# Kernel optimization log

Measured on AMD Instinct MI355X. Metric: run time of the kernel, lower is better.

The kernel has to match this reference:

```python
import jax, jax.numpy as jnp
import numpy as np


def setup_inputs() -> dict:
    key = jax.random.key(0)
    ks = jax.random.split(key, 20)
    B, T, N, Cin = 1, 12, 30000, 16
    H, Hc = 64, 128
    O, KW = 12, 128
    E2 = 480000  # half of edges; symmetrized below -> E = 960000
    s = 0.05
    node_features = jax.random.normal(ks[0], (B, T, N, Cin), jnp.float32)
    src = jax.random.randint(ks[1], (T, E2), 0, N)
    dst = jax.random.randint(ks[2], (T, E2), 0, N)
    edge_index = jnp.concatenate(
        [jnp.stack([src, dst], axis=1), jnp.stack([dst, src], axis=1)], axis=-1)  # [T,2,E]
    return dict(
        node_features=node_features,
        edge_index=edge_index,
        gru_Wih0=jax.random.normal(ks[3], (2, 3 * H, Cin), jnp.float32) * s,
        gru_Whh0=jax.random.normal(ks[4], (2, 3 * H, H), jnp.float32) * s,
        gru_bih0=jax.random.normal(ks[5], (2, 3 * H), jnp.float32) * s,
        gru_bhh0=jax.random.normal(ks[6], (2, 3 * H), jnp.float32) * s,
        gru_Wih1=jax.random.normal(ks[7], (2, 3 * H, 2 * H), jnp.float32) * s,
        gru_Whh1=jax.random.normal(ks[8], (2, 3 * H, H), jnp.float32) * s,
        gru_bih1=jax.random.normal(ks[9], (2, 3 * H), jnp.float32) * s,
        gru_bhh1=jax.random.normal(ks[10], (2, 3 * H), jnp.float32) * s,
        ln_scale=jnp.ones((H,), jnp.float32),
        ln_bias=jnp.zeros((H,), jnp.float32),
        cheb_W=jax.random.normal(ks[11], (3, H, Hc), jnp.float32) * s,
        cheb_b=jnp.zeros((Hc,), jnp.float32),
        conv_W=jax.random.normal(ks[12], (O, T, 1, KW), jnp.float32) * s,
        conv_b=jnp.zeros((O,), jnp.float32),
    )


def reference(node_features, edge_index, gru_Wih0, gru_Whh0, gru_bih0, gru_bhh0,
              gru_Wih1, gru_Whh1, gru_bih1, gru_bhh1, ln_scale, ln_bias,
              cheb_W, cheb_b, conv_W, conv_b):
    B, T, N, Cin = node_features.shape
    H = gru_Whh0.shape[-1]
    M = B * N
    x = node_features.transpose(0, 2, 1, 3).reshape(M, T, Cin)

    def bigru(x, Wih, Whh, bih, bhh):
        # PyTorch bidirectional GRU layer (eval mode -> no dropout)
        outs = []
        for d, rev in ((0, False), (1, True)):
            gi = jnp.einsum('mtd,gd->tmg', x, Wih[d]) + bih[d]  # [T, M, 3H]
            def step(h, g, d=d):
                gh = h @ Whh[d].T + bhh[d]
                ir, iz, inn = jnp.split(g, 3, axis=-1)
                hr, hz, hn = jnp.split(gh, 3, axis=-1)
                r = jax.nn.sigmoid(ir + hr)
                z = jax.nn.sigmoid(iz + hz)
                n = jnp.tanh(inn + r * hn)
                h = (1.0 - z) * n + z * h
                return h, h
            h0 = jnp.zeros((x.shape[0], Whh.shape[-1]), x.dtype)
            _, ys = jax.lax.scan(step, h0, gi, reverse=rev)
            outs.append(jnp.swapaxes(ys, 0, 1))
        return jnp.concatenate(outs, axis=-1)  # [M, T, 2H]

    x = bigru(x, gru_Wih0, gru_Whh0, gru_bih0, gru_bhh0)
    x = bigru(x, gru_Wih1, gru_Whh1, gru_bih1, gru_bhh1)
    # reshape(M,T,2,H), LayerNorm(H), take direction 1 == slice then LayerNorm
    xb = x[:, :, H:]
    mu = jnp.mean(xb, axis=-1, keepdims=True)
    var = jnp.mean((xb - mu) ** 2, axis=-1, keepdims=True)
    xb = (xb - mu) * jax.lax.rsqrt(var + 1e-5) * ln_scale + ln_bias
    xs_t = jnp.moveaxis(xb.reshape(B, N, T, H), 2, 0).reshape(T, M, H)  # per-timestep [M,H]

    E = edge_index.shape[-1]
    N_ITER = 75  # power-iteration steps for lambda_max (scipy eigs equivalent)

    def cheb_step(_, inp):
        x_t, edges = inp  # x_t [M,H], edges [2,E]
        row, col = edges[0], edges[1]
        deg = jax.ops.segment_sum(jnp.ones((E,), x_t.dtype), row, num_segments=M)
        def Lmv(v):  # unnormalized Laplacian (D - A) matvec
            return deg * v - jax.ops.segment_sum(v[col], row, num_segments=M)
        v0 = jnp.full((M,), 1.0 / np.sqrt(M), x_t.dtype)
        def pit(i, v):
            w = Lmv(v)
            return w / (jnp.linalg.norm(w) + 1e-12)
        v = jax.lax.fori_loop(0, N_ITER, pit, v0)
        lam = jnp.vdot(v, Lmv(v))  # lambda_max of D - A (LaplacianLambdaMax default)
        # ChebConv sym-normalized, rescaled Laplacian: L_hat = (2/lam)*(I - D^-1/2 A D^-1/2) - I
        dinv = jnp.where(deg > 0, 1.0 / jnp.sqrt(jnp.maximum(deg, 1.0)), 0.0)
        we = (-2.0 / lam) * dinv[row] * dinv[col]  # off-diagonal weights
        diag = 2.0 / lam - 1.0                      # diagonal (all nodes)
        def Lhat(xm):
            return diag * xm + jax.ops.segment_sum(we[:, None] * xm[col], row, num_segments=M)
        Tx0 = x_t
        Tx1 = Lhat(Tx0)
        Tx2 = 2.0 * Lhat(Tx1) - Tx0
        out = Tx0 @ cheb_W[0] + Tx1 @ cheb_W[1] + Tx2 @ cheb_W[2] + cheb_b
        return 0, out

    _, emb = jax.lax.scan(cheb_step, 0, (xs_t, edge_index))  # [T, M, Hc]
    Hc = cheb_W.shape[-1]
    emb = jnp.moveaxis(emb.reshape(T, B, N, Hc), 0, 1)  # [B, T, N, Hc]
    # Conv2d(T -> O, kernel (1,KW)) followed by [:,:,:,-1]: only last window matters
    KW = conv_W.shape[-1]
    out = jnp.einsum('btnk,otk->bno', emb[..., Hc - KW:], conv_W[:, :, 0, :]) + conv_b
    return jax.nn.sigmoid(out)  # [B, N, num_for_predict]
```

## Files before the change

kernel.cpp:

```cpp
#include <hip/hip_runtime.h>
#include <hip/hip_bf16.h>

#define DEV __device__ __forceinline__

constexpr int Mn  = 30000;
constexpr int Tt  = 12;
constexpr int CIN = 16;
constexpr int Hh  = 64;
constexpr int Gg  = 192;
constexpr int C2  = 128;
constexpr int Ee  = 960000;
constexpr int HC  = 128;
constexpr int Oo  = 12;
constexpr int KW  = 128;
constexpr int SEGS= 938;
constexpr int NB  = 235;
constexpr int EPB = 8192;
constexpr int BPT = 118;
constexpr int CHK = 21;
constexpr int RC  = 1440;
constexpr int NRND= 76;
constexpr int NF4A= 21*256;
constexpr int NF4B= 20*104 + 44;

DEV float bf2f(__hip_bfloat16 v){ return __bfloat162float(v); }
DEV __hip_bfloat16 f2bf(float v){ return __float2bfloat16(v); }
DEV float sigm(float x){ return __builtin_amdgcn_rcpf(1.f + __expf(-x)); }
DEV float tanh_f(float x){ return 1.f - 2.f*__builtin_amdgcn_rcpf(__expf(2.f*x) + 1.f); }

DEV float aload_f(const float* p){ return __hip_atomic_load(p, __ATOMIC_RELAXED, __HIP_MEMORY_SCOPE_AGENT); }
DEV void  astore_f(float* p, float v){ __hip_atomic_store(p, v, __ATOMIC_RELAXED, __HIP_MEMORY_SCOPE_AGENT); }
DEV int   aload_i(const int* p){ return __hip_atomic_load(p, __ATOMIC_RELAXED, __HIP_MEMORY_SCOPE_AGENT); }
DEV void  astore_i(int* p, int v){ __hip_atomic_store(p, v, __ATOMIC_RELAXED, __HIP_MEMORY_SCOPE_AGENT); }
DEV unsigned long long aload_u64(const unsigned long long* p){ return __hip_atomic_load(p, __ATOMIC_RELAXED, __HIP_MEMORY_SCOPE_AGENT); }
DEV void astore_u64(unsigned long long* p, unsigned long long v){ __hip_atomic_store(p, v, __ATOMIC_RELAXED, __HIP_MEMORY_SCOPE_AGENT); }

typedef short bfrag8 __attribute__((ext_vector_type(8)));
typedef float ffrag4 __attribute__((ext_vector_type(4)));

DEV int off_h(int row, int col){
  return row*64 + ((((col >> 3) ^ (row & 7)) << 3) | (col & 7));
}

DEV short bfbits(float v){ __hip_bfloat16 b = f2bf(v); return *reinterpret_cast<short*>(&b); }

__global__ void k_init(int* bcnt, int* bfill, int* flagA, unsigned long long* pbB){
  int i = blockIdx.x*256 + threadIdx.x;
  if (i < Tt*CHK*16){ flagA[i] = 0; pbB[i] = 0ull; }
  if (i < Tt*NB){ bcnt[i] = 0; bfill[i] = 0; }
}

__global__ __launch_bounds__(256) void k_bcnt(const int* __restrict__ ei, int* __restrict__ bcnt){
  __shared__ int h[NB];
  const int b = blockIdx.x;
  const int w = (b & 7)*177 + (b >> 3);
  const int t = w / BPT, ch = w - t*BPT;
  const int e0 = ch*EPB;
  const int tid = threadIdx.x;
  for (int i = tid; i < NB; i += 256) h[i] = 0;
  __syncthreads();
  #pragma unroll
  for (int i = 0; i < 32; ++i){
    int e = e0 + i*256 + tid;
    if (e < Ee){
      int r = ei[(size_t)(t*2)*Ee + e];
      atomicAdd(&h[r >> 7], 1);
    }
  }
  __syncthreads();
  for (int i = tid; i < NB; i += 256){
    int c = h[i];
    if (c > 0) atomicAdd(&bcnt[t*NB + i], c);
  }
}

__global__ __launch_bounds__(256) void k_bscan(const int* __restrict__ bcnt, int* __restrict__ rpb){
  int t = blockIdx.x, tid = threadIdx.x;
  __shared__ int ps[256];
  int v = (tid < NB) ? bcnt[t*NB + tid] : 0;
  ps[tid] = v;
  __syncthreads();
  for (int o = 1; o < 256; o <<= 1){
    int x = (tid >= o) ? ps[tid-o] : 0;
    __syncthreads();
    ps[tid] += x;
    __syncthreads();
  }
  if (tid < NB) rpb[t*(NB+1) + tid] = ps[tid] - v;
  if (tid == 255) rpb[t*(NB+1) + NB] = ps[NB-1];
}

__global__ __launch_bounds__(256) void k_part2(const int* __restrict__ ei, const int* __restrict__ rpb,
    int* __restrict__ bfill, unsigned* __restrict__ pair){
  __shared__ int hcnt[NB];
  __shared__ int hbase[NB];
  const int b = blockIdx.x;
  const int w = (b & 7)*177 + (b >> 3);
  const int t = w / BPT, ch = w - t*BPT;
  const int e0 = ch*EPB;
  const int tid = threadIdx.x;
  for (int i = tid; i < NB; i += 256) hcnt[i] = 0;
  __syncthreads();
  unsigned key[32];
  #pragma unroll
  for (int i = 0; i < 32; ++i){
    int e = e0 + i*256 + tid;
    unsigned k = 0xFFFFFFFFu;
    if (e < Ee){
      int r = ei[(size_t)(t*2)*Ee + e];
      int c = ei[(size_t)(t*2+1)*Ee + e];
      k = ((unsigned)r << 16) | (unsigned)c;
      atomicAdd(&hcnt[r >> 7], 1);
    }
    key[i] = k;
  }
  __syncthreads();
  for (int i = tid; i < NB; i += 256){
    int cnt = hcnt[i];
    int base = (cnt > 0) ? atomicAdd(&bfill[t*NB + i], cnt) : 0;
    hbase[i] = rpb[t*(NB+1) + i] + base;
  }
  __syncthreads();
  for (int i = tid; i < NB; i += 256) hcnt[i] = 0;
  __syncthreads();
  #pragma unroll
  for (int i = 0; i < 32; ++i){
    unsigned k = key[i];
    if (k != 0xFFFFFFFFu){
      int r = (int)(k >> 16);
      int bk = r >> 7;
      int pos = atomicAdd(&hcnt[bk], 1);
      pair[(size_t)t*Ee + hbase[bk] + pos] = ((unsigned)(r & 127) << 16) | (k & 0xFFFFu);
    }
  }
}

__global__ __launch_bounds__(256) void k_csr2(const int* __restrict__ rpb, const unsigned* __restrict__ pair,
    unsigned short* __restrict__ col16, int* __restrict__ rp, float* __restrict__ dinv){
  __shared__ unsigned short cols_s[9216];
  __shared__ int lcnt[128], lfill[128];
  __shared__ int ps[256];
  const int blk = blockIdx.x;
  const int t = blk / NB, bk = blk - t*NB;
  const int r0 = bk << 7;
  const int nr = (r0 + 128 <= Mn) ? 128 : (Mn - r0);
  const int base = rpb[t*(NB+1) + bk];
  const int cnt  = rpb[t*(NB+1) + bk + 1] - base;
  const int tid = threadIdx.x;
  if (tid < 128) lcnt[tid] = 0;
  __syncthreads();
  for (int i = tid; i < cnt; i += 256){
    unsigned v = pair[(size_t)t*Ee + base + i];
    atomicAdd(&lcnt[v >> 16], 1);
  }
  __syncthreads();
  int v2 = (tid < 128) ? lcnt[tid] : 0;
  ps[tid] = v2;
  __syncthreads();
  for (int o = 1; o < 128; o <<= 1){
    int x = (tid >= o) ? ps[tid-o] : 0;
    __syncthreads();
    ps[tid] += x;
    __syncthreads();
  }
  if (tid < 128){
    int excl = ps[tid] - v2;
    lfill[tid] = excl;
    if (tid < nr){
      rp[t*(Mn+1) + r0 + tid] = base + excl;
      dinv[t*Mn + r0 + tid] = (v2 > 0) ? rsqrtf((float)v2) : 0.f;
    }
  }
  if (bk == NB-1 && tid == 0) rp[t*(Mn+1) + Mn] = base + cnt;
  __syncthreads();
  for (int i = tid; i < cnt; i += 256){
    unsigned v = pair[(size_t)t*Ee + base + i];
    int pos = atomicAdd(&lfill[v >> 16], 1);
    cols_s[pos] = (unsigned short)(v & 0xFFFFu);
  }
  __syncthreads();
  for (int i = tid; i < cnt; i += 256)
    col16[(size_t)t*Ee + base + i] = cols_s[i];
}

__global__ __launch_bounds__(1024) void k_perm(const int* __restrict__ rp, int* __restrict__ prow){
  __shared__ int hist[256], hbase[256], ps[256];
  const int b = blockIdx.x;
  const int t = b / CHK, ch = b - t*CHK;
  const int r0 = ch*RC;
  const int r1 = (r0 + RC < Mn) ? r0 + RC : Mn;
  const int n = r1 - r0;
  const int tid = threadIdx.x;
  if (tid < 256) hist[tid] = 0;
  __syncthreads();
  const int* rpt = rp + t*(Mn+1);
  int d0 = -1, d1 = -1;
  if (tid < n){ int m = r0 + tid; d0 = min(rpt[m+1]-rpt[m], 255); atomicAdd(&hist[d0], 1); }
  if (1024 + tid < n){ int m = r0 + 1024 + tid; d1 = min(rpt[m+1]-rpt[m], 255); atomicAdd(&hist[d1], 1); }
  __syncthreads();
  if (tid < 256) ps[tid] = hist[tid];
  __syncthreads();
  for (int o = 1; o < 256; o <<= 1){
    int x = (tid >= o && tid < 256) ? ps[tid-o] : 0;
    __syncthreads();
    if (tid < 256) ps[tid] += x;
    __syncthreads();
  }
  if (tid < 256){ hbase[tid] = ps[tid] - hist[tid]; hist[tid] = 0; }
  __syncthreads();
  if (d0 >= 0){ int pos = hbase[d0] + atomicAdd(&hist[d0], 1); prow[(size_t)b*RC + pos] = r0 + tid; }
  if (d1 >= 0){ int pos = hbase[d1] + atomicAdd(&hist[d1], 1); prow[(size_t)b*RC + pos] = r0 + 1024 + tid; }
}

__global__ __launch_bounds__(256) void k_gru0(
    const float* __restrict__ nf, const float* __restrict__ Wih, const float* __restrict__ Whh,
    const float* __restrict__ bih, const float* __restrict__ bhh, __hip_bfloat16* __restrict__ y0)
{
  __shared__ __hip_bfloat16 xp[Tt*32*32];
  __shared__ __hip_bfloat16 h_hi[32*64];
  __shared__ __hip_bfloat16 h_lo[32*64];
  const int tid = threadIdx.x;
  const int m0  = blockIdx.x*32;
  const int lane = tid & 63, wv = tid >> 6;
  const int lr = lane & 15, lq = lane >> 4;
  for (int idx = tid; idx < Tt*32*CIN; idx += 256){
    int t = idx >> 9; int row = (idx >> 4) & 31; int k = idx & 15;
    int m = m0 + row;
    float v = (m < Mn) ? nf[((size_t)t*Mn + m)*CIN + k] : 0.f;
    __hip_bfloat16 hi = f2bf(v);
    xp[(t*32 + row)*32 + k]      = hi;
    xp[(t*32 + row)*32 + 16 + k] = f2bf(v - bf2f(hi));
  }
  for (int d = 0; d < 2; ++d){
    bfrag8 Bh[3][2], Bx[3];
    float b_r, b_z, b_in, b_hn;
    {
      const float* Wh = Whh + (size_t)d*Gg*Hh;
      const float* Wx = Wih + (size_t)d*Gg*CIN;
      #pragma unroll
      for (int c = 0; c < 3; ++c){
        int g = (wv + 4*c)*16 + lr;
        #pragma unroll
        for (int ks = 0; ks < 2; ++ks){
          bfrag8 f;
          #pragma unroll
          for (int r = 0; r < 8; ++r) f[r] = bfbits(Wh[(size_t)g*Hh + ks*32 + lq*8 + r]);
          Bh[c][ks] = f;
        }
        bfrag8 fx;
        #pragma unroll
        for (int r = 0; r < 8; ++r) fx[r] = bfbits(Wx[(size_t)g*CIN + ((lq*8 + r) & 15)]);
        Bx[c] = fx;
      }
      int j = wv*16 + lr;
      b_r  = bih[d*Gg + j]        + bhh[d*Gg + j];
      b_z  = bih[d*Gg + Hh + j]   + bhh[d*Gg + Hh + j];
      b_in = bih[d*Gg + 2*Hh + j];
      b_hn = bhh[d*Gg + 2*Hh + j];
    }
    float hreg[8];
    #pragma unroll
    for (int q = 0; q < 8; ++q) hreg[q] = 0.f;
    for (int i = tid; i < 32*64; i += 256){ h_hi[i] = f2bf(0.f); h_lo[i] = f2bf(0.f); }
    __syncthreads();
    for (int step = 0; step < Tt; ++step){
      int t = d ? (Tt-1-step) : step;
      bfrag8 xa[2], hhf[2][2], hlf[2][2];
      #pragma unroll
      for (int rt = 0; rt < 2; ++rt){
        int row = rt*16 + lr;
        xa[rt] = *(const bfrag8*)&xp[(t*32 + row)*32 + lq*8];
        #pragma unroll
        for (int ks = 0; ks < 2; ++ks){
          int e = off_h(row, ks*32 + lq*8);
          hhf[rt][ks] = *(const bfrag8*)&h_hi[e];
          hlf[rt][ks] = *(const bfrag8*)&h_lo[e];
        }
      }
      ffrag4 Cr[2], Cz[2], Cai[2], Cah[2];
      #pragma unroll
      for (int rt = 0; rt < 2; ++rt){
        ffrag4 z4 = (ffrag4){0.f,0.f,0.f,0.f};
        Cr[rt]  = __builtin_amdgcn_mfma_f32_16x16x32_bf16(xa[rt], Bx[0], z4, 0,0,0);
        Cz[rt]  = __builtin_amdgcn_mfma_f32_16x16x32_bf16(xa[rt], Bx[1], z4, 0,0,0);
        Cai[rt] = __builtin_amdgcn_mfma_f32_16x16x32_bf16(xa[rt], Bx[2], z4, 0,0,0);
        Cah[rt] = z4;
        #pragma unroll
        for (int ks = 0; ks < 2; ++ks){
          Cr[rt]  = __builtin_amdgcn_mfma_f32_16x16x32_bf16(hhf[rt][ks], Bh[0][ks], Cr[rt], 0,0,0);
          Cr[rt]  = __builtin_amdgcn_mfma_f32_16x16x32_bf16(hlf[rt][ks], Bh[0][ks], Cr[rt], 0,0,0);
          Cz[rt]  = __builtin_amdgcn_mfma_f32_16x16x32_bf16(hhf[rt][ks], Bh[1][ks], Cz[rt], 0,0,0);
          Cz[rt]  = __builtin_amdgcn_mfma_f32_16x16x32_bf16(hlf[rt][ks], Bh[1][ks], Cz[rt], 0,0,0);
          Cah[rt] = __builtin_amdgcn_mfma_f32_16x16x32_bf16(hhf[rt][ks], Bh[2][ks], Cah[rt], 0,0,0);
          Cah[rt] = __builtin_amdgcn_mfma_f32_16x16x32_bf16(hlf[rt][ks], Bh[2][ks], Cah[rt], 0,0,0);
        }
      }
      __syncthreads();
      #pragma unroll
      for (int rt = 0; rt < 2; ++rt){
        #pragma unroll
        for (int q = 0; q < 4; ++q){
          float r = sigm(Cr[rt][q] + b_r);
          float z = sigm(Cz[rt][q] + b_z);
          float n = tanh_f((Cai[rt][q] + b_in) + r*(Cah[rt][q] + b_hn));
          float h = (1.f - z)*n + z*hreg[rt*4+q];
          hreg[rt*4+q] = h;
          __hip_bfloat16 hi = f2bf(h);
          int e = off_h(rt*16 + lq*4 + q, wv*16 + lr);
          h_hi[e] = hi;
          h_lo[e] = f2bf(h - bf2f(hi));
        }
      }
      __syncthreads();
      {
        int row = tid >> 3, cg = tid & 7;
        int m = m0 + row;
        if (m < Mn){
          float4 v = *(const float4*)&h_hi[off_h(row, cg*8)];
          *(float4*)&y0[((size_t)t*Mn + m)*C2 + d*Hh + cg*8] = v;
        }
      }
    }
    __syncthreads();
  }
}

__global__ void k_wcvt(const float* __restrict__ W, __hip_bfloat16* __restrict__ Wbf){
  int i = blockIdx.x*256 + threadIdx.x;
  if (i < Gg*C2) Wbf[i] = f2bf(W[i]);
}

__global__ __launch_bounds__(256) void k_gru1r(const __hip_bfloat16* __restrict__ y0,
    const __hip_bfloat16* __restrict__ Wbf, const float* __restrict__ Whh,
    const float* __restrict__ bih, const float* __restrict__ bhh,
    const float* __restrict__ lns, const float* __restrict__ lnb,
    __hip_bfloat16* __restrict__ xbt)
{
  __shared__ __hip_bfloat16 h_hi[32*64];
  __shared__ __hip_bfloat16 h_lo[32*64];
  __shared__ float h_f32[32*72];
  __shared__ float sc[Hh], bs[Hh];
  const int tid = threadIdx.x;
  const int seg = blockIdx.x;
  const int m0  = seg*32;
  const int lane = tid & 63, wv = tid >> 6;
  const int lr = lane & 15, lq = lane >> 4;
  bfrag8 Bh[3][2];
  #pragma unroll
  for (int c = 0; c < 3; ++c){
    int g = (wv + 4*c)*16 + lr;
    #pragma unroll
    for (int ks = 0; ks < 2; ++ks){
      bfrag8 f;
      #pragma unroll
      for (int r = 0; r < 8; ++r) f[r] = bfbits(Whh[(size_t)g*Hh + ks*32 + lq*8 + r]);
      Bh[c][ks] = f;
    }
  }
  bfrag8 Bp[3][4];
  #pragma unroll
  for (int c = 0; c < 3; ++c){
    int g = (wv + 4*c)*16 + lr;
    #pragma unroll
    for (int ks = 0; ks < 4; ++ks)
      Bp[c][ks] = *(const bfrag8*)(Wbf + (size_t)g*C2 + ks*32 + lq*8);
  }
  float b_r, b_z, b_in, b_hn;
  {
    int j = wv*16 + lr;
    b_r  = bih[j]      + bhh[j];
    b_z  = bih[Hh+j]   + bhh[Hh+j];
    b_in = bih[2*Hh+j];
    b_hn = bhh[2*Hh+j];
  }
  if (tid < Hh){ sc[tid] = lns[tid]; bs[tid] = lnb[tid]; }
  float hreg[8];
  #pragma unroll
  for (int q = 0; q < 8; ++q) hreg[q] = 0.f;
  for (int i = tid; i < 32*64; i += 256){ h_hi[i] = f2bf(0.f); h_lo[i] = f2bf(0.f); }
  __syncthreads();
  for (int step = 0; step < Tt; ++step){
    int t = Tt-1-step;
    const __hip_bfloat16* yb = y0 + (size_t)t*Mn*C2;
    ffrag4 Cr[2], Cz[2], Cai[2], Cah[2];
    #pragma unroll
    for (int rt = 0; rt < 2; ++rt){
      ffrag4 z4 = (ffrag4){0.f,0.f,0.f,0.f};
      Cr[rt] = z4; Cz[rt] = z4; Cai[rt] = z4; Cah[rt] = z4;
    }
    #pragma unroll
    for (int ks = 0; ks < 4; ++ks){
      const int ko = ks*32 + lq*8;
      bfrag8 a0 = *(const bfrag8*)(yb + (size_t)(m0 + lr     )*C2 + ko);
      bfrag8 a1 = *(const bfrag8*)(yb + (size_t)(m0 + 16 + lr)*C2 + ko);
      Cr[0]  = __builtin_amdgcn_mfma_f32_16x16x32_bf16(a0, Bp[0][ks], Cr[0], 0,0,0);
      Cr[1]  = __builtin_amdgcn_mfma_f32_16x16x32_bf16(a1, Bp[0][ks], Cr[1], 0,0,0);
      Cz[0]  = __builtin_amdgcn_mfma_f32_16x16x32_bf16(a0, Bp[1][ks], Cz[0], 0,0,0);
      Cz[1]  = __builtin_amdgcn_mfma_f32_16x16x32_bf16(a1, Bp[1][ks], Cz[1], 0,0,0);
      Cai[0] = __builtin_amdgcn_mfma_f32_16x16x32_bf16(a0, Bp[2][ks], Cai[0], 0,0,0);
      Cai[1] = __builtin_amdgcn_mfma_f32_16x16x32_bf16(a1, Bp[2][ks], Cai[1], 0,0,0);
    }
    bfrag8 hhf[2][2], hlf[2][2];
    #pragma unroll
    for (int rt = 0; rt < 2; ++rt){
      int row = rt*16 + lr;
      #pragma unroll
      for (int ks = 0; ks < 2; ++ks){
        int e = off_h(row, ks*32 + lq*8);
        hhf[rt][ks] = *(const bfrag8*)&h_hi[e];
        hlf[rt][ks] = *(const bfrag8*)&h_lo[e];
      }
    }
    #pragma unroll
    for (int rt = 0; rt < 2; ++rt){
      #pragma unroll
      for (int ks = 0; ks < 2; ++ks){
        Cr[rt]  = __builtin_amdgcn_mfma_f32_16x16x32_bf16(hhf[rt][ks], Bh[0][ks], Cr[rt], 0,0,0);
        Cr[rt]  = __builtin_amdgcn_mfma_f32_16x16x32_bf16(hlf[rt][ks], Bh[0][ks], Cr[rt], 0,0,0);
        Cz[rt]  = __builtin_amdgcn_mfma_f32_16x16x32_bf16(hhf[rt][ks], Bh[1][ks], Cz[rt], 0,0,0);
        Cz[rt]  = __builtin_amdgcn_mfma_f32_16x16x32_bf16(hlf[rt][ks], Bh[1][ks], Cz[rt], 0,0,0);
        Cah[rt] = __builtin_amdgcn_mfma_f32_16x16x32_bf16(hhf[rt][ks], Bh[2][ks], Cah[rt], 0,0,0);
        Cah[rt] = __builtin_amdgcn_mfma_f32_16x16x32_bf16(hlf[rt][ks], Bh[2][ks], Cah[rt], 0,0,0);
      }
    }
    __syncthreads();
    #pragma unroll
    for (int rt = 0; rt < 2; ++rt){
      #pragma unroll
      for (int q = 0; q < 4; ++q){
        float r = sigm(Cr[rt][q] + b_r);
        float z = sigm(Cz[rt][q] + b_z);
        float n = tanh_f((Cai[rt][q] + b_in) + r*(Cah[rt][q] + b_hn));
        float h = (1.f - z)*n + z*hreg[rt*4+q];
        hreg[rt*4+q] = h;
        __hip_bfloat16 hi = f2bf(h);
        int row = rt*16 + lq*4 + q;
        int e = off_h(row, wv*16 + lr);
        h_hi[e] = hi;
        h_lo[e] = f2bf(h - bf2f(hi));
        h_f32[row*72 + wv*16 + lr] = h;
      }
    }
    __syncthreads();
    {
      int row = tid >> 3, l = tid & 7;
      float4 v0 = *(const float4*)&h_f32[row*72 + l*8];
      float4 v1 = *(const float4*)&h_f32[row*72 + l*8 + 4];
      float vals[8] = {v0.x, v0.y, v0.z, v0.w, v1.x, v1.y, v1.z, v1.w};
      float s1 = 0.f, s2 = 0.f;
      #pragma unroll
      for (int q = 0; q < 8; ++q){ s1 += vals[q]; s2 += vals[q]*vals[q]; }
      #pragma unroll
      for (int off = 1; off <= 4; off <<= 1){ s1 += __shfl_xor(s1, off); s2 += __shfl_xor(s2, off); }
      float mu  = s1 * (1.f/64.f);
      float var = s2 * (1.f/64.f) - mu*mu;
      float rs  = rsqrtf(var + 1e-5f);
      int m = m0 + row;
      if (m < Mn){
        __hip_bfloat16 ob[8];
        #pragma unroll
        for (int q = 0; q < 8; ++q){ int j = l*8 + q; ob[q] = f2bf((vals[q]-mu)*rs*sc[j] + bs[j]); }
        *(float4*)&xbt[((size_t)t*Mn + m)*Hh + l*8] = *(float4*)ob;
      }
    }
    __syncthreads();
  }
}

__global__ __launch_bounds__(1024) void k_pitall(const int* __restrict__ rp,
    const unsigned short* __restrict__ col, float* __restrict__ urb,
    int* __restrict__ flagA, unsigned long long* __restrict__ pbB,
    float* __restrict__ lamc, const int* __restrict__ prow, int rA, int rB)
{
  __shared__ alignas(16) float u_s[Mn];
  __shared__ float redw[16];
  __shared__ float s_nrm;
  __shared__ int s_goA, s_goB;
  const int b = blockIdx.x;
  const int t = b / CHK, ch = b - t*CHK;
  const int r0 = ch*RC;
  const int r1 = (r0 + RC < Mn) ? r0 + RC : Mn;
  const int n = r1 - r0;
  const int tid = threadIdx.x;
  const int lane = tid & 63;
  const int wv   = tid >> 6;
  const unsigned short* cp = col + (size_t)t*Ee;
  const int fS = t*CHK*16;
  const int pB = t*CHK*16;
  const int* pr = prow + (size_t)b*RC;
  const int rowA = (tid < n)        ? pr[tid]        : -1;
  const int rowB = (1024 + tid < n) ? pr[1024 + tid] : -1;
  int rb0 = 0, re0 = 0, rb1 = 0, re1 = 0;
  {
    const int* rpt = rp + t*(Mn+1);
    if (rowA >= 0){ rb0 = rpt[rowA]; re0 = rpt[rowA+1]; }
    if (rowB >= 0){ rb1 = rpt[rowB]; re1 = rpt[rowB+1]; }
  }
  if (tid == 0){ s_nrm = 1.0f; s_goA = 0; s_goB = 0; }
  __syncthreads();
  for (int r = rA; r <= rB; ++r){
    const int fin = (r == NRND);
    if (r == 1){
      for (int i = tid; i < Mn; i += 1024) u_s[i] = 0.005773502691896258f;
    } else {
      const int rr = r - 1;
      const float4* u4 = (const float4*)(urb + (size_t)rr*(Tt*Mn) + (size_t)t*Mn);
      float4* s4 = (float4*)u_s;
      if (wv == 0){
        const bool mine = lane < CHK;
        for (;;){ int v = mine ? aload_i(&flagA[fS + lane*16]) : 0x7FFFFFFF;
                  if (__all(v >= rr)) break; __builtin_amdgcn_s_sleep(4); }
        if (lane == 0) __hip_atomic_store(&s_goA, rr, __ATOMIC_RELAXED, __HIP_MEMORY_SCOPE_WORKGROUP);
      } else {
        while (__hip_atomic_load(&s_goA, __ATOMIC_RELAXED, __HIP_MEMORY_SCOPE_WORKGROUP) < rr)
          __builtin_amdgcn_s_sleep(2);
      }
      asm volatile("" ::: "memory");
      for (int i = tid; i < NF4A; i += 1024){
        int idx = (i >> 8)*360 + (i & 255);
        s4[idx] = u4[idx];
      }
      unsigned long long pv = 0;
      if (wv == 0){
        const bool mine = lane < CHK;
        for (;;){ pv = mine ? aload_u64(&pbB[(size_t)(pB + lane*16) + (rr & 1)*8])
                            : ((unsigned long long)rr << 32);
                  if (__all((int)(pv >> 32) == rr)) break; __builtin_amdgcn_s_sleep(4); }
        if (lane == 0) __hip_atomic_store(&s_goB, rr, __ATOMIC_RELAXED, __HIP_MEMORY_SCOPE_WORKGROUP);
      } else {
        while (__hip_atomic_load(&s_goB, __ATOMIC_RELAXED, __HIP_MEMORY_SCOPE_WORKGROUP) < rr)
          __builtin_amdgcn_s_sleep(2);
      }
      asm volatile("" ::: "memory");
      for (int i = tid; i < NF4B; i += 1024){
        int ck = i/104, off = i - ck*104;
        int idx = ck*360 + 256 + off;
        s4[idx] = u4[idx];
      }
      if (wv == 0){
        float p = (lane < CHK) ? __uint_as_float((unsigned)pv) : 0.f;
        #pragma unroll
        for (int o2 = 1; o2 < 32; o2 <<= 1) p += __shfl_xor(p, o2);
        if (tid == 0) s_nrm = p;
      }
    }
    __syncthreads();
    const float inv_s = fin ? 1.f : 1.f/(sqrtf(s_nrm) + 1e-12f);
    float* u_ot = urb + (size_t)r*(Tt*Mn);
    float local = 0.f;
    if (rowA >= 0){
      float s = 0.f;
      int i = rb0;
      for (; i < re0 && (i & 3); ++i) s += u_s[cp[i]];
      for (; i + 4 <= re0; i += 4){
        ushort4 c4 = *(const ushort4*)(cp + i);
        s += (u_s[c4.x] + u_s[c4.y]) + (u_s[c4.z] + u_s[c4.w]);
      }
      for (; i < re0; ++i) s += u_s[cp[i]];
      float uv = u_s[rowA];
      float wv2 = (float)(re0 - rb0)*uv - s;
      if (!fin){ float o = inv_s*wv2; astore_f(&u_ot[t*Mn + rowA], o); local += o*o; }
      else local += uv*wv2;
    }
    asm volatile("s_waitcnt vmcnt(0)" ::: "memory");
    __syncthreads();
    if (tid == 0) astore_i(&flagA[fS + ch*16], r);
    if (rowB >= 0){
      float s = 0.f;
      int i = rb1;
      for (; i < re1 && (i & 3); ++i) s += u_s[cp[i]];
      for (; i + 4 <= re1; i += 4){
        ushort4 c4 = *(const ushort4*)(cp + i);
        s += (u_s[c4.x] + u_s[c4.y]) + (u_s[c4.z] + u_s[c4.w]);
      }
      for (; i < re1; ++i) s += u_s[cp[i]];
      float uv = u_s[rowB];
      float wv2 = (float)(re1 - rb1)*uv - s;
      if (!fin){ float o = inv_s*wv2; astore_f(&u_ot[t*Mn + rowB], o); local += o*o; }
      else local += uv*wv2;
    }
    #pragma unroll
    for (int o2 = 1; o2 < 64; o2 <<= 1) local += __shfl_xor(local, o2);
    if ((tid & 63) == 0) redw[tid >> 6] = local;
    asm volatile("s_waitcnt vmcnt(0)" ::: "memory");
    __syncthreads();
    if (tid < 64){
      float tot = (tid < 16) ? redw[tid] : 0.f;
      #pragma unroll
      for (int o2 = 1; o2 < 16; o2 <<= 1) tot += __shfl_xor(tot, o2);
      if (tid == 0){
        unsigned long long out = ((unsigned long long)r << 32)
                               | (unsigned long long)__float_as_uint(tot);
        astore_u64(&pbB[(size_t)(pB + ch*16) + (r & 1)*8], out);
      }
    }
  }
  if (rB == NRND && ch == 0 && tid < 64){
    const bool mine = lane < CHK;
    unsigned long long pv = 0;
    for (;;){ pv = mine ? aload_u64(&pbB[(size_t)(pB + lane*16) + (NRND & 1)*8])
                        : ((unsigned long long)NRND << 32);
              if (__all((int)(pv >> 32) == NRND)) break; __builtin_amdgcn_s_sleep(4); }
    float p = mine ? __uint_as_float((unsigned)pv) : 0.f;
    #pragma unroll
    for (int o2 = 1; o2 < 32; o2 <<= 1) p += __shfl_xor(p, o2);
    if (tid == 0){
      float nn = sqrtf(s_nrm) + 1e-12f;
      float lam = p / (nn*nn);
      lamc[2*t+0] = -2.f/lam;
      lamc[2*t+1] =  2.f/lam - 1.f;
    }
  }
}

__global__ __launch_bounds__(256) void k_cheb(const __hip_bfloat16* __restrict__ xin,
    const __hip_bfloat16* __restrict__ xb0, __hip_bfloat16* __restrict__ outp,
    const int* __restrict__ rp, const unsigned short* __restrict__ col,
    const float* __restrict__ dinv, const float* __restrict__ lamc, float s1, float s2)
{
  const int blk = blockIdx.x;
  const int w = (blk & 7)*11250 + (blk >> 3);
  const int gw = w*4 + (threadIdx.x >> 6);
  const int lane = threadIdx.x & 63;
  int t = gw / Mn, m = gw - t*Mn;
  float coef = lamc[2*t], diag = lamc[2*t+1];
  const __hip_bfloat16* xt = xin + (size_t)t*Mn*Hh;
  const float* dv = dinv + t*Mn;
  float acc = diag * bf2f(xt[(size_t)m*Hh + lane]);
  float cdm = coef * dv[m];
  int bgn = rp[t*(Mn+1)+m], end = rp[t*(Mn+1)+m+1];
  const unsigned short* cp = col + (size_t)t*Ee;
  int i = bgn;
  for (; i < end && (i & 3); ++i){ int c = cp[i]; acc += (cdm*dv[c])*bf2f(xt[(size_t)c*Hh + lane]); }
  for (; i + 4 <= end; i += 4){
    ushort4 c4 = *(const ushort4*)(cp + i);
    float w0 = cdm*dv[c4.x], w1 = cdm*dv[c4.y], w2 = cdm*dv[c4.z], w3 = cdm*dv[c4.w];
    acc += w0*bf2f(xt[(size_t)c4.x*Hh + lane]);
    acc += w1*bf2f(xt[(size_t)c4.y*Hh + lane]);
    acc += w2*bf2f(xt[(size_t)c4.z*Hh + lane]);
    acc += w3*bf2f(xt[(size_t)c4.w*Hh + lane]);
  }
  for (; i < end; ++i){ int c = cp[i]; acc += (cdm*dv[c])*bf2f(xt[(size_t)c*Hh + lane]); }
  float o = s1*acc;
  if (s2 != 0.f) o += s2*bf2f(xb0[(size_t)gw*Hh + lane]);
  outp[(size_t)gw*Hh + lane] = f2bf(o);
}

__global__ void k_ww(const float* __restrict__ chebW, const float* __restrict__ chebb,
    const float* __restrict__ convW, const float* __restrict__ convb, float* __restrict__ WW, float* __restrict__ c0)
{
  int idx = blockIdx.x*256 + threadIdx.x;
  if (idx < 3*Tt*Hh*Oo){
    int oc = idx % Oo; int j = (idx/Oo) % Hh; int t = (idx/(Oo*Hh)) % Tt; int i = idx/(Oo*Hh*Tt);
    const float* cw = chebW + ((size_t)i*Hh + j)*HC + (HC-KW);
    const float* vw = convW + ((size_t)oc*Tt + t)*KW;
    float s = 0.f;
    for (int k = 0; k < KW; ++k) s += cw[k]*vw[k];
    WW[idx] = s;
  }
  if (blockIdx.x == 0 && threadIdx.x < Oo){
    int oc = threadIdx.x;
    float s = convb[oc];
    for (int t = 0; t < Tt; ++t){
      const float* vw = convW + ((size_t)oc*Tt + t)*KW;
      for (int k = 0; k < KW; ++k) s += chebb[(HC-KW)+k]*vw[k];
    }
    c0[oc] = s;
  }
}

__global__ __launch_bounds__(256) void k_final(const __hip_bfloat16* __restrict__ tx0,
    const __hip_bfloat16* __restrict__ tx1, const __hip_bfloat16* __restrict__ tx2,
    const float* __restrict__ WW, const float* __restrict__ c0, float* __restrict__ outp)
{
  __shared__ float xs[64][65];
  __shared__ float ww[64][12];
  const int tid = threadIdx.x;
  const int n0 = blockIdx.x*64;
  const int n = tid & 63, ob = (tid >> 6)*3;
  float acc[3] = {0.f, 0.f, 0.f};
  for (int it = 0; it < 3*Tt; ++it){
    int ii = it / Tt, t = it % Tt;
    const __hip_bfloat16* tx = (ii == 0) ? tx0 : (ii == 1) ? tx1 : tx2;
    __syncthreads();
    for (int idx = tid; idx < 64*64; idx += 256){
      int mm = idx >> 6, j = idx & 63;
      int m = n0 + mm;
      xs[mm][j] = (m < Mn) ? bf2f(tx[((size_t)t*Mn + m)*Hh + j]) : 0.f;
    }
    for (int idx = tid; idx < 64*Oo; idx += 256)
      ((float*)ww)[idx] = WW[((size_t)(ii*Tt + t)*Hh)*Oo + idx];
    __syncthreads();
    #pragma unroll 8
    for (int j = 0; j < 64; ++j){
      float x = xs[n][j];
      acc[0] += x*ww[j][ob+0];
      acc[1] += x*ww[j][ob+1];
      acc[2] += x*ww[j][ob+2];
    }
  }
  int m = n0 + n;
  if (m < Mn){
    #pragma unroll
    for (int q = 0; q < 3; ++q) outp[(size_t)m*Oo + ob + q] = sigm(acc[q] + c0[ob+q]);
  }
}

extern "C" void kernel_launch(void* const* d_in, const int* in_sizes, int n_in,
                              void* d_out, int out_size, void* d_ws, size_t ws_size,
                              hipStream_t stream)
{
  const float* nf    = (const float*)d_in[0];
  const int*   ei    = (const int*)d_in[1];
  const float* Wih0  = (const float*)d_in[2];
  const float* Whh0  = (const float*)d_in[3];
  const float* bih0  = (const float*)d_in[4];
  const float* bhh0  = (const float*)d_in[5];
  const float* Wih1  = (const float*)d_in[6];
  const float* Whh1  = (const float*)d_in[7];
  const float* bih1  = (const float*)d_in[8];
  const float* bhh1  = (const float*)d_in[9];
  const float* lns   = (const float*)d_in[10];
  const float* lnb   = (const float*)d_in[11];
  const float* chebW = (const float*)d_in[12];
  const float* chebb = (const float*)d_in[13];
  const float* convW = (const float*)d_in[14];
  const float* convb = (const float*)d_in[15];
  float* outp = (float*)d_out;

  char* base = (char*)d_ws;
  size_t off = 0;
  auto alloc = [&](size_t bytes)->char*{ char* p = base + off; off += (bytes + 255) & ~(size_t)255; return p; };

  __hip_bfloat16* y0  = (__hip_bfloat16*)alloc((size_t)Tt*Mn*C2*2);
  __hip_bfloat16* tx1 = y0;
  __hip_bfloat16* tx2 = y0 + (size_t)Tt*Mn*Hh;
  char* arena = alloc((size_t)(NRND+1)*Tt*Mn*4);
  unsigned* pair = (unsigned*)arena;
  float*    urb  = (float*)arena;
  __hip_bfloat16* xbt = (__hip_bfloat16*)alloc((size_t)Tt*Mn*Hh*2);
  unsigned short* col16 = (unsigned short*)alloc((size_t)Tt*Ee*2);
  int*   rp   = (int*)alloc((size_t)Tt*(Mn+1)*4);
  int*   bcnt = (int*)alloc((size_t)Tt*NB*4);
  int*   bfill= (int*)alloc((size_t)Tt*NB*4);
  int*   rpb  = (int*)alloc((size_t)Tt*(NB+1)*4);
  float* dinv = (float*)alloc((size_t)Tt*Mn*4);
  float* lamc = (float*)alloc((size_t)2*Tt*4);
  float* WW   = (float*)alloc((size_t)3*Tt*Hh*Oo*4);
  float* c0   = (float*)alloc((size_t)Oo*4);
  __hip_bfloat16* Wbf = (__hip_bfloat16*)alloc((size_t)Gg*C2*2);
  int*   flagA = (int*)alloc((size_t)Tt*CHK*16*4);
  unsigned long long* pbB = (unsigned long long*)alloc((size_t)Tt*CHK*16*8);
  int*   prow = (int*)alloc((size_t)Tt*CHK*RC*4);
  (void)ws_size; (void)in_sizes; (void)n_in; (void)out_size;

  k_init<<<16, 256, 0, stream>>>(bcnt, bfill, flagA, pbB);
  k_bcnt<<<Tt*BPT, 256, 0, stream>>>(ei, bcnt);
  k_bscan<<<Tt, 256, 0, stream>>>(bcnt, rpb);
  k_part2<<<Tt*BPT, 256, 0, stream>>>(ei, rpb, bfill, pair);
  k_csr2<<<Tt*NB, 256, 0, stream>>>(rpb, pair, col16, rp, dinv);
  k_perm<<<Tt*CHK, 1024, 0, stream>>>(rp, prow);

  k_wcvt<<<(Gg*C2 + 255)/256, 256, 0, stream>>>(Wih1 + (size_t)Gg*C2, Wbf);
  k_gru0<<<SEGS, 256, 0, stream>>>(nf, Wih0, Whh0, bih0, bhh0, y0);
  k_gru1r<<<SEGS, 256, 0, stream>>>(y0, Wbf, Whh1 + (size_t)Gg*Hh,
                                    bih1 + Gg, bhh1 + Gg, lns, lnb, xbt);

  k_pitall<<<Tt*CHK, 1024, 0, stream>>>(rp, col16, urb, flagA, pbB, lamc, prow, 1, 38);
  k_pitall<<<Tt*CHK, 1024, 0, stream>>>(rp, col16, urb, flagA, pbB, lamc, prow, 39, NRND);

  k_cheb<<<(Tt*Mn)/4, 256, 0, stream>>>(xbt, xbt, tx1, rp, col16, dinv, lamc, 1.f, 0.f);
  k_cheb<<<(Tt*Mn)/4, 256, 0, stream>>>(tx1, xbt, tx2, rp, col16, dinv, lamc, 2.f, -1.f);

  k_ww<<<(3*Tt*Hh*Oo + 255)/256, 256, 0, stream>>>(chebW, chebb, convW, convb, WW, c0);
  k_final<<<(Mn + 63)/64, 256, 0, stream>>>(xbt, tx1, tx2, WW, c0, outp);
}
```

Before: 2.846 ms.

## Renumber power-iteration vector in degree-sorted order and merge launches

Adds an inverse permutation map and a remap kernel that rewrites CSR column indices into the degree-sorted row order. The power-iteration vector is then stored and indexed in permuted space, so each thread writes contiguous outputs and reads its own entry without indirection. The two split power-iteration launches are merged into one. This costs an extra remap pass and a second column array, and the single persistent launch relies on all blocks being co-resident for the spin-wait synchronisation.

```diff
diff --git a/kernel.cpp b/kernel.cpp
--- a/kernel.cpp
+++ b/kernel.cpp
@@ -19,9 +19,10 @@
 constexpr int BPT = 118;
 constexpr int CHK = 21;
 constexpr int RC  = 1440;
+constexpr int UP  = CHK*RC;
 constexpr int NRND= 76;
 constexpr int NF4A= 21*256;
-constexpr int NF4B= 20*104 + 44;
+constexpr int NF4B= 21*104;
 
 DEV float bf2f(__hip_bfloat16 v){ return __bfloat162float(v); }
 DEV __hip_bfloat16 f2bf(float v){ return __float2bfloat16(v); }
@@ -183,7 +184,8 @@
     col16[(size_t)t*Ee + base + i] = cols_s[i];
 }
 
-__global__ __launch_bounds__(1024) void k_perm(const int* __restrict__ rp, int* __restrict__ prow){
+__global__ __launch_bounds__(1024) void k_perm(const int* __restrict__ rp,
+    int* __restrict__ prow, int* __restrict__ imap){
   __shared__ int hist[256], hbase[256], ps[256];
   const int b = blockIdx.x;
   const int t = b / CHK, ch = b - t*CHK;
@@ -208,8 +210,30 @@
   }
   if (tid < 256){ hbase[tid] = ps[tid] - hist[tid]; hist[tid] = 0; }
   __syncthreads();
-  if (d0 >= 0){ int pos = hbase[d0] + atomicAdd(&hist[d0], 1); prow[(size_t)b*RC + pos] = r0 + tid; }
-  if (d1 >= 0){ int pos = hbase[d1] + atomicAdd(&hist[d1], 1); prow[(size_t)b*RC + pos] = r0 + 1024 + tid; }
+  if (d0 >= 0){
+    int pos = hbase[d0] + atomicAdd(&hist[d0], 1);
+    prow[(size_t)b*RC + pos] = r0 + tid;
+    imap[t*Mn + r0 + tid] = ch*RC + pos;
+  }
+  if (d1 >= 0){
+    int pos = hbase[d1] + atomicAdd(&hist[d1], 1);
+    prow[(size_t)b*RC + pos] = r0 + 1024 + tid;
+    imap[t*Mn + r0 + 1024 + tid] = ch*RC + pos;
+  }
+}
+
+__global__ __launch_bounds__(256) void k_remap(const unsigned short* __restrict__ col16,
+    const int* __restrict__ imap, unsigned short* __restrict__ colp){
+  const size_t total4 = (size_t)Tt*Ee/4;
+  for (size_t i = (size_t)blockIdx.x*256 + threadIdx.x; i < total4; i += (size_t)gridDim.x*256){
+    int t = (int)((i*4) / Ee);
+    const int* mp = imap + (size_t)t*Mn;
+    ushort4 c = ((const ushort4*)col16)[i];
+    ushort4 o;
+    o.x = (unsigned short)mp[c.x]; o.y = (unsigned short)mp[c.y];
+    o.z = (unsigned short)mp[c.z]; o.w = (unsigned short)mp[c.w];
+    ((ushort4*)colp)[i] = o;
+  }
 }
 
 __global__ __launch_bounds__(256) void k_gru0(
@@ -468,43 +492,44 @@
 }
 
 __global__ __launch_bounds__(1024) void k_pitall(const int* __restrict__ rp,
-    const unsigned short* __restrict__ col, float* __restrict__ urb,
+    const unsigned short* __restrict__ colp, float* __restrict__ urb,
     int* __restrict__ flagA, unsigned long long* __restrict__ pbB,
-    float* __restrict__ lamc, const int* __restrict__ prow, int rA, int rB)
+    float* __restrict__ lamc, const int* __restrict__ prow)
 {
-  __shared__ alignas(16) float u_s[Mn];
+  __shared__ alignas(16) float u_s[UP];
   __shared__ float redw[16];
   __shared__ float s_nrm;
   __shared__ int s_goA, s_goB;
   const int b = blockIdx.x;
   const int t = b / CHK, ch = b - t*CHK;
   const int r0 = ch*RC;
-  const int r1 = (r0 + RC < Mn) ? r0 + RC : Mn;
-  const int n = r1 - r0;
+  const int n = (r0 + RC < Mn) ? RC : (Mn - r0);
   const int tid = threadIdx.x;
   const int lane = tid & 63;
   const int wv   = tid >> 6;
-  const unsigned short* cp = col + (size_t)t*Ee;
+  const unsigned short* cp = colp + (size_t)t*Ee;
   const int fS = t*CHK*16;
-  const int pB = t*CHK*16;
-  const int* pr = prow + (size_t)b*RC;
-  const int rowA = (tid < n)        ? pr[tid]        : -1;
-  const int rowB = (1024 + tid < n) ? pr[1024 + tid] : -1;
+  const int pS = t*CHK*16;
+  const int posA = tid, posB = 1024 + tid;
+  const int rowA = prow[(size_t)b*RC + posA];
+  const int rowB = (posB < n) ? prow[(size_t)b*RC + posB] : -1;
+  const int newA = ch*RC + posA;
+  const int newB = ch*RC + posB;
   int rb0 = 0, re0 = 0, rb1 = 0, re1 = 0;
   {
     const int* rpt = rp + t*(Mn+1);
-    if (rowA >= 0){ rb0 = rpt[rowA]; re0 = rpt[rowA+1]; }
+    rb0 = rpt[rowA]; re0 = rpt[rowA+1];
     if (rowB >= 0){ rb1 = rpt[rowB]; re1 = rpt[rowB+1]; }
   }
   if (tid == 0){ s_nrm = 1.0f; s_goA = 0; s_goB = 0; }
   __syncthreads();
-  for (int r = rA; r <= rB; ++r){
+  for (int r = 1; r <= NRND; ++r){
     const int fin = (r == NRND);
     if (r == 1){
-      for (int i = tid; i < Mn; i += 1024) u_s[i] = 0.005773502691896258f;
+      for (int i = tid; i < UP; i += 1024) u_s[i] = 0.005773502691896258f;
     } else {
       const int rr = r - 1;
-      const float4* u4 = (const float4*)(urb + (size_t)rr*(Tt*Mn) + (size_t)t*Mn);
+      const float4* u4 = (const float4*)(urb + (size_t)rr*(Tt*UP) + (size_t)t*UP);
       float4* s4 = (float4*)u_s;
       if (wv == 0){
         const bool mine = lane < CHK;
@@ -523,7 +548,7 @@
       unsigned long long pv = 0;
       if (wv == 0){
         const bool mine = lane < CHK;
-        for (;;){ pv = mine ? aload_u64(&pbB[(size_t)(pB + lane*16) + (rr & 1)*8])
+        for (;;){ pv = mine ? aload_u64(&pbB[(size_t)(pS + lane*16) + (rr & 1)*8])
                             : ((unsigned long long)rr << 32);
                   if (__all((int)(pv >> 32) == rr)) break; __builtin_amdgcn_s_sleep(4); }
         if (lane == 0) __hip_atomic_store(&s_goB, rr, __ATOMIC_RELAXED, __HIP_MEMORY_SCOPE_WORKGROUP);
@@ -546,9 +571,9 @@
     }
     __syncthreads();
     const float inv_s = fin ? 1.f : 1.f/(sqrtf(s_nrm) + 1e-12f);
-    float* u_ot = urb + (size_t)r*(Tt*Mn);
+    float* u_ot = urb + (size_t)r*(Tt*UP) + (size_t)t*UP;
     float local = 0.f;
-    if (rowA >= 0){
+    {
       float s = 0.f;
       int i = rb0;
       for (; i < re0 && (i & 3); ++i) s += u_s[cp[i]];
@@ -557,9 +582,9 @@
         s += (u_s[c4.x] + u_s[c4.y]) + (u_s[c4.z] + u_s[c4.w]);
       }
       for (; i < re0; ++i) s += u_s[cp[i]];
-      float uv = u_s[rowA];
+      float uv = u_s[newA];
       float wv2 = (float)(re0 - rb0)*uv - s;
-      if (!fin){ float o = inv_s*wv2; astore_f(&u_ot[t*Mn + rowA], o); local += o*o; }
+      if (!fin){ float o = inv_s*wv2; astore_f(&u_ot[newA], o); local += o*o; }
       else local += uv*wv2;
     }
     asm volatile("s_waitcnt vmcnt(0)" ::: "memory");
@@ -574,9 +599,9 @@
         s += (u_s[c4.x] + u_s[c4.y]) + (u_s[c4.z] + u_s[c4.w]);
       }
       for (; i < re1; ++i) s += u_s[cp[i]];
-      float uv = u_s[rowB];
+      float uv = u_s[newB];
       float wv2 = (float)(re1 - rb1)*uv - s;
-      if (!fin){ float o = inv_s*wv2; astore_f(&u_ot[t*Mn + rowB], o); local += o*o; }
+      if (!fin){ float o = inv_s*wv2; astore_f(&u_ot[newB], o); local += o*o; }
       else local += uv*wv2;
     }
     #pragma unroll
@@ -591,14 +616,14 @@
       if (tid == 0){
         unsigned long long out = ((unsigned long long)r << 32)
                                | (unsigned long long)__float_as_uint(tot);
-        astore_u64(&pbB[(size_t)(pB + ch*16) + (r & 1)*8], out);
-      }
-    }
-  }
-  if (rB == NRND && ch == 0 && tid < 64){
+        astore_u64(&pbB[(size_t)(pS + ch*16) + (r & 1)*8], out);
+      }
+    }
+  }
+  if (ch == 0 && tid < 64){
     const bool mine = lane < CHK;
     unsigned long long pv = 0;
-    for (;;){ pv = mine ? aload_u64(&pbB[(size_t)(pB + lane*16) + (NRND & 1)*8])
+    for (;;){ pv = mine ? aload_u64(&pbB[(size_t)(pS + lane*16) + (NRND & 1)*8])
                         : ((unsigned long long)NRND << 32);
               if (__all((int)(pv >> 32) == NRND)) break; __builtin_amdgcn_s_sleep(4); }
     float p = mine ? __uint_as_float((unsigned)pv) : 0.f;
@@ -735,11 +760,12 @@
   __hip_bfloat16* y0  = (__hip_bfloat16*)alloc((size_t)Tt*Mn*C2*2);
   __hip_bfloat16* tx1 = y0;
   __hip_bfloat16* tx2 = y0 + (size_t)Tt*Mn*Hh;
-  char* arena = alloc((size_t)(NRND+1)*Tt*Mn*4);
+  char* arena = alloc((size_t)(NRND+1)*Tt*UP*4);
   unsigned* pair = (unsigned*)arena;
   float*    urb  = (float*)arena;
   __hip_bfloat16* xbt = (__hip_bfloat16*)alloc((size_t)Tt*Mn*Hh*2);
   unsigned short* col16 = (unsigned short*)alloc((size_t)Tt*Ee*2);
+  unsigned short* colp  = (unsigned short*)alloc((size_t)Tt*Ee*2);
   int*   rp   = (int*)alloc((size_t)Tt*(Mn+1)*4);
   int*   bcnt = (int*)alloc((size_t)Tt*NB*4);
   int*   bfill= (int*)alloc((size_t)Tt*NB*4);
@@ -752,6 +778,7 @@
   int*   flagA = (int*)alloc((size_t)Tt*CHK*16*4);
   unsigned long long* pbB = (unsigned long long*)alloc((size_t)Tt*CHK*16*8);
   int*   prow = (int*)alloc((size_t)Tt*CHK*RC*4);
+  int*   imap = (int*)alloc((size_t)Tt*Mn*4);
   (void)ws_size; (void)in_sizes; (void)n_in; (void)out_size;
 
   k_init<<<16, 256, 0, stream>>>(bcnt, bfill, flagA, pbB);
@@ -759,15 +786,15 @@
   k_bscan<<<Tt, 256, 0, stream>>>(bcnt, rpb);
   k_part2<<<Tt*BPT, 256, 0, stream>>>(ei, rpb, bfill, pair);
   k_csr2<<<Tt*NB, 256, 0, stream>>>(rpb, pair, col16, rp, dinv);
-  k_perm<<<Tt*CHK, 1024, 0, stream>>>(rp, prow);
+  k_perm<<<Tt*CHK, 1024, 0, stream>>>(rp, prow, imap);
+  k_remap<<<2048, 256, 0, stream>>>(col16, imap, colp);
 
   k_wcvt<<<(Gg*C2 + 255)/256, 256, 0, stream>>>(Wih1 + (size_t)Gg*C2, Wbf);
   k_gru0<<<SEGS, 256, 0, stream>>>(nf, Wih0, Whh0, bih0, bhh0, y0);
   k_gru1r<<<SEGS, 256, 0, stream>>>(y0, Wbf, Whh1 + (size_t)Gg*Hh,
                                     bih1 + Gg, bhh1 + Gg, lns, lnb, xbt);
 
-  k_pitall<<<Tt*CHK, 1024, 0, stream>>>(rp, col16, urb, flagA, pbB, lamc, prow, 1, 38);
-  k_pitall<<<Tt*CHK, 1024, 0, stream>>>(rp, col16, urb, flagA, pbB, lamc, prow, 39, NRND);
+  k_pitall<<<Tt*CHK, 1024, 0, stream>>>(rp, colp, urb, flagA, pbB, lamc, prow);
 
   k_cheb<<<(Tt*Mn)/4, 256, 0, stream>>>(xbt, xbt, tx1, rp, col16, dinv, lamc, 1.f, 0.f);
   k_cheb<<<(Tt*Mn)/4, 256, 0, stream>>>(tx1, xbt, tx2, rp, col16, dinv, lamc, 2.f, -1.f);
```

Result: no change. 2.795 ms (-1.8%).
